# Kernel tuning notes

Measured on AMD Instinct MI355X. Metric: run time of the kernel, lower is better.

The kernel has to match this reference:

```python
import jax, jax.numpy as jnp
import numpy as np

POOL_H, POOL_W = 7, 7


def _crop_and_resize_one(feat, boxes, pool_h, pool_w):
    """TF crop_and_resize-style bilinear sampling.
    feat: [H, W, C]; boxes: [N, 4] normalized (y1, x1, y2, x2).
    Returns [N, pool_h, pool_w, C].
    """
    H, W, C = feat.shape
    y1, x1, y2, x2 = boxes[:, 0], boxes[:, 1], boxes[:, 2], boxes[:, 3]
    fy = jnp.arange(pool_h, dtype=feat.dtype) / (pool_h - 1)  # [ph] in [0,1]
    fx = jnp.arange(pool_w, dtype=feat.dtype) / (pool_w - 1)  # [pw]
    ys = (y1[:, None] + fy[None, :] * (y2 - y1)[:, None]) * (H - 1)  # [N, ph]
    xs = (x1[:, None] + fx[None, :] * (x2 - x1)[:, None]) * (W - 1)  # [N, pw]
    y0f = jnp.clip(jnp.floor(ys), 0, H - 1)
    x0f = jnp.clip(jnp.floor(xs), 0, W - 1)
    y0 = y0f.astype(jnp.int32)
    x0 = x0f.astype(jnp.int32)
    y1i = jnp.clip(y0 + 1, 0, H - 1)
    x1i = jnp.clip(x0 + 1, 0, W - 1)
    wy = (ys - y0f)[:, :, None, None]  # [N, ph, 1, 1]
    wx = (xs - x0f)[:, None, :, None]  # [N, 1, pw, 1]
    # four corner gathers -> [N, ph, pw, C]
    f00 = feat[y0[:, :, None], x0[:, None, :]]
    f01 = feat[y0[:, :, None], x1i[:, None, :]]
    f10 = feat[y1i[:, :, None], x0[:, None, :]]
    f11 = feat[y1i[:, :, None], x1i[:, None, :]]
    top = f00 + (f01 - f00) * wx
    bot = f10 + (f11 - f10) * wx
    return top + (bot - top) * wy


def setup_inputs() -> dict:
    key = jax.random.key(0)
    kf, kb = jax.random.split(key)
    B, H, W, C, N = 2, 64, 64, 256, 2000
    features = jax.random.normal(kf, (B, H, W, C), dtype=jnp.float32)
    p = jax.random.uniform(kb, (B, N, 4), dtype=jnp.float32)
    # ensure valid normalized boxes (y1<=y2, x1<=x2)
    rois = jnp.stack([
        jnp.minimum(p[..., 0], p[..., 2]),
        jnp.minimum(p[..., 1], p[..., 3]),
        jnp.maximum(p[..., 0], p[..., 2]),
        jnp.maximum(p[..., 1], p[..., 3]),
    ], axis=-1)
    return {"features": features, "rois": rois}


def reference(features, rois):
    # [B, N, 7, 7, C]
    return jax.vmap(lambda f, b: _crop_and_resize_one(f, b, POOL_H, POOL_W))(features, rois)
```

## Files before the change

### kernel.cpp

```cpp
#include <hip/hip_runtime.h>


#define POOL  7
#define NBINS 128
#define CAP   14000
#define BPB   8

typedef float vfloat4 __attribute__((ext_vector_type(4)));

__global__ void zero_counts(int* __restrict__ counts) {
    if ((int)threadIdx.x < NBINS) counts[threadIdx.x] = 0;
}

__global__ __launch_bounds__(256) void bin_rows(
    const float* __restrict__ rois,
    int* __restrict__ counts,
    int* __restrict__ slots,
    int H, int N)
{
    const int rows_per_batch = N * POOL;
    const int total = 2 * rows_per_batch;
    const int gid = blockIdx.x * 256 + threadIdx.x;
    if (gid >= total) return;

    const int b   = gid / rows_per_batch;
    const int rem = gid - b * rows_per_batch;
    const int n   = rem / POOL;
    const int py  = rem - n * POOL;

    const float* r = rois + ((long long)b * N + n) * 4;
    const float ry1 = r[0], ry2 = r[2];

    const float fy  = (float)py * (1.0f / (POOL - 1));
    const float ys  = (ry1 + fy * (ry2 - ry1)) * (float)(H - 1);
    const float y0f = fminf(fmaxf(floorf(ys), 0.0f), (float)(H - 1));
    const int   y0  = (int)y0f;

    const int bin = b * 64 + y0;
    const int idx = atomicAdd(&counts[bin], 1);
    slots[bin * CAP + idx] = rem;
}

__global__ __launch_bounds__(1024) void roialign_binned(
    const float* __restrict__ feat,
    const float* __restrict__ rois,
    float* __restrict__ out,
    const int* __restrict__ counts,
    const int* __restrict__ slots,
    int H, int W, int C4, int N)
{
    __shared__ vfloat4 lds[2][64 * 64];

    const int bin = blockIdx.x >> 3;
    const int j   = blockIdx.x & (BPB - 1);
    const int count = counts[bin];
    const int s0 = (j * count) / BPB;
    const int s1 = ((j + 1) * count) / BPB;
    if (s0 >= s1) return;

    const int b   = bin >> 6;
    const int y0  = bin & 63;
    const int y1i = min(y0 + 1, H - 1);

    const vfloat4* fb = (const vfloat4*)feat + (long long)b * H * W * C4;
    const vfloat4* g0 = fb + (long long)y0  * W * C4;
    const vfloat4* g1 = fb + (long long)y1i * W * C4;
    for (int t = threadIdx.x; t < W * C4; t += 1024) {
        lds[0][t] = g0[t];
        lds[1][t] = g1[t];
    }
    __syncthreads();

    const int lane = threadIdx.x & 63;
    const int wid  = threadIdx.x >> 6;

    for (int i = s0 + wid; i < s1; i += 16) {
        const int rem = slots[bin * CAP + i];
        const int n   = rem / POOL;
        const int py  = rem - n * POOL;

        const float* r = rois + ((long long)b * N + n) * 4;
        const float ry1 = r[0], rx1 = r[1], ry2 = r[2], rx2 = r[3];

        const float fy  = (float)py * (1.0f / (POOL - 1));
        const float ys  = (ry1 + fy * (ry2 - ry1)) * (float)(H - 1);
        const float y0f = fminf(fmaxf(floorf(ys), 0.0f), (float)(H - 1));
        const float wy  = ys - y0f;
        const float dx  = rx2 - rx1;

        vfloat4* ob = (vfloat4*)out +
            (((long long)b * N + n) * (POOL * POOL) + (long long)py * POOL) * C4 + lane;

#pragma unroll
        for (int px = 0; px < POOL; ++px) {
            const float fx  = (float)px * (1.0f / (POOL - 1));
            const float xs  = (rx1 + fx * dx) * (float)(W - 1);
            const float x0f = fminf(fmaxf(floorf(xs), 0.0f), (float)(W - 1));
            const int   x0  = (int)x0f;
            const int   x1i = min(x0 + 1, W - 1);
            const float wx  = xs - x0f;

            const vfloat4 f00 = lds[0][x0  * C4 + lane];
            const vfloat4 f01 = lds[0][x1i * C4 + lane];
            const vfloat4 f10 = lds[1][x0  * C4 + lane];
            const vfloat4 f11 = lds[1][x1i * C4 + lane];

            const vfloat4 top = f00 + (f01 - f00) * wx;
            const vfloat4 bot = f10 + (f11 - f10) * wx;
            const vfloat4 o   = top + (bot - top) * wy;

            __builtin_nontemporal_store(o, ob + px * C4);
        }
    }
}

__global__ __launch_bounds__(256) void roialign_direct(
    const float* __restrict__ feat, const float* __restrict__ rois,
    float* __restrict__ out, int H, int W, int C4, int N, int blocks_per_batch)
{
    const int lane = threadIdx.x & 63;
    const int wid  = threadIdx.x >> 6;
    const int xcd  = blockIdx.x & 7;
    const int slot = blockIdx.x >> 3;
    const int b    = xcd >> 2;
    const int lblock = slot * 4 + (xcd & 3);
    if (lblock >= blocks_per_batch) return;
    const int row = lblock * 4 + wid;
    if (row >= N * POOL) return;
    const int n  = row / POOL;
    const int py = row - n * POOL;

    const float* r = rois + ((long long)b * N + n) * 4;
    const float ry1 = r[0], rx1 = r[1], ry2 = r[2], rx2 = r[3];
    const float fy  = (float)py * (1.0f / (POOL - 1));
    const float ys  = (ry1 + fy * (ry2 - ry1)) * (float)(H - 1);
    const float y0f = fminf(fmaxf(floorf(ys), 0.0f), (float)(H - 1));
    const int   y0  = (int)y0f;
    const int   y1i = min(y0 + 1, H - 1);
    const float wy  = ys - y0f;

    const vfloat4* fb = (const vfloat4*)feat + (long long)b * H * W * C4;
    const vfloat4* r0 = fb + (long long)y0  * W * C4 + lane;
    const vfloat4* r1 = fb + (long long)y1i * W * C4 + lane;
    vfloat4* ob = (vfloat4*)out +
        (((long long)b * N + n) * (POOL * POOL) + (long long)py * POOL) * C4 + lane;
    const float dx = rx2 - rx1;
#pragma unroll
    for (int px = 0; px < POOL; ++px) {
        const float fx  = (float)px * (1.0f / (POOL - 1));
        const float xs  = (rx1 + fx * dx) * (float)(W - 1);
        const float x0f = fminf(fmaxf(floorf(xs), 0.0f), (float)(W - 1));
        const int   x0  = (int)x0f;
        const int   x1i = min(x0 + 1, W - 1);
        const float wx  = xs - x0f;
        const vfloat4 f00 = r0[x0  * C4];
        const vfloat4 f01 = r0[x1i * C4];
        const vfloat4 f10 = r1[x0  * C4];
        const vfloat4 f11 = r1[x1i * C4];
        const vfloat4 top = f00 + (f01 - f00) * wx;
        const vfloat4 bot = f10 + (f11 - f10) * wx;
        const vfloat4 o   = top + (bot - top) * wy;
        __builtin_nontemporal_store(o, ob + px * C4);
    }
}

extern "C" void kernel_launch(void* const* d_in, const int* in_sizes, int n_in,
                              void* d_out, int out_size, void* d_ws, size_t ws_size,
                              hipStream_t stream) {
    const int B = 2, H = 64, W = 64, C = 256;
    const int N = in_sizes[1] / (B * 4);

    const float* feat = (const float*)d_in[0];
    const float* rois = (const float*)d_in[1];
    float* out = (float*)d_out;

    const size_t ws_needed = (size_t)NBINS * 4
                           + (size_t)NBINS * CAP * 4;

    if (ws_size >= ws_needed && d_ws != nullptr) {
        int* counts = (int*)d_ws;
        int* slots  = counts + NBINS;

        const int total_rows = B * N * POOL;
        const int bin_blocks = (total_rows + 255) / 256;

        zero_counts<<<1, NBINS, 0, stream>>>(counts);
        bin_rows<<<bin_blocks, 256, 0, stream>>>(rois, counts, slots, H, N);
        roialign_binned<<<NBINS * BPB, 1024, 0, stream>>>(
            feat, rois, out, counts, slots, H, W, C / 4, N);
    } else {
        const int rows_per_batch   = N * POOL;
        const int blocks_per_batch = (rows_per_batch + 3) / 4;
        const int slots_g  = (blocks_per_batch + 3) / 4;
        roialign_direct<<<slots_g * 8, 256, 0, stream>>>(
            feat, rois, out, H, W, C / 4, N, blocks_per_batch);
    }
}
```

Baseline: 245.3 us.

## Replace LDS-staged binned kernel with sorted-row global-gather kernel via prefix scan

Drops the per-bin LDS staging of two feature rows. Each wavefront now handles one output row, found through a prefix-scanned offset table and a binary search over bins, so rows that share a y0 run next to each other and hit the same feature rows in L2. A 40 KB dummy shared array caps occupancy, presumably to keep concurrent wavefronts on nearby bins. The cost is an extra scan kernel plus a binary search per wave, in exchange for removing the LDS load phase and the load imbalance across bins.

```diff
diff --git a/kernel.cpp b/kernel.cpp
--- a/kernel.cpp
+++ b/kernel.cpp
@@ -3,8 +3,6 @@
 
 #define POOL  7
 #define NBINS 128
-#define CAP   14000
-#define BPB   8
 
 typedef float vfloat4 __attribute__((ext_vector_type(4)));
 
@@ -16,7 +14,7 @@
     const float* __restrict__ rois,
     int* __restrict__ counts,
     int* __restrict__ slots,
-    int H, int N)
+    int H, int N, int CAP)
 {
     const int rows_per_batch = N * POOL;
     const int total = 2 * rows_per_batch;
@@ -41,76 +39,88 @@
     slots[bin * CAP + idx] = rem;
 }
 
-__global__ __launch_bounds__(1024) void roialign_binned(
+__global__ void prefix_scan(const int* __restrict__ counts,
+                            int* __restrict__ offsets) {
+    __shared__ int tmp[NBINS];
+    const int t = threadIdx.x;
+    tmp[t] = counts[t];
+    __syncthreads();
+    for (int d = 1; d < NBINS; d <<= 1) {
+        const int v = (t >= d) ? tmp[t - d] : 0;
+        __syncthreads();
+        tmp[t] += v;
+        __syncthreads();
+    }
+    offsets[t + 1] = tmp[t];
+    if (t == 0) offsets[0] = 0;
+}
+
+__global__ __launch_bounds__(256) void roialign_sorted(
     const float* __restrict__ feat,
     const float* __restrict__ rois,
     float* __restrict__ out,
-    const int* __restrict__ counts,
+    const int* __restrict__ offsets,
     const int* __restrict__ slots,
-    int H, int W, int C4, int N)
+    int H, int W, int C4, int N, int CAP, int total)
 {
-    __shared__ vfloat4 lds[2][64 * 64];
-
-    const int bin = blockIdx.x >> 3;
-    const int j   = blockIdx.x & (BPB - 1);
-    const int count = counts[bin];
-    const int s0 = (j * count) / BPB;
-    const int s1 = ((j + 1) * count) / BPB;
-    if (s0 >= s1) return;
-
-    const int b   = bin >> 6;
-    const int y0  = bin & 63;
-    const int y1i = min(y0 + 1, H - 1);
-
-    const vfloat4* fb = (const vfloat4*)feat + (long long)b * H * W * C4;
-    const vfloat4* g0 = fb + (long long)y0  * W * C4;
-    const vfloat4* g1 = fb + (long long)y1i * W * C4;
-    for (int t = threadIdx.x; t < W * C4; t += 1024) {
-        lds[0][t] = g0[t];
-        lds[1][t] = g1[t];
-    }
-    __syncthreads();
+    __shared__ int occ_pad[10240];
+    if (H == 0) ((volatile int*)occ_pad)[threadIdx.x] = 1;
 
     const int lane = threadIdx.x & 63;
     const int wid  = threadIdx.x >> 6;
-
-    for (int i = s0 + wid; i < s1; i += 16) {
-        const int rem = slots[bin * CAP + i];
-        const int n   = rem / POOL;
-        const int py  = rem - n * POOL;
-
-        const float* r = rois + ((long long)b * N + n) * 4;
-        const float ry1 = r[0], rx1 = r[1], ry2 = r[2], rx2 = r[3];
-
-        const float fy  = (float)py * (1.0f / (POOL - 1));
-        const float ys  = (ry1 + fy * (ry2 - ry1)) * (float)(H - 1);
-        const float y0f = fminf(fmaxf(floorf(ys), 0.0f), (float)(H - 1));
-        const float wy  = ys - y0f;
-        const float dx  = rx2 - rx1;
-
-        vfloat4* ob = (vfloat4*)out +
-            (((long long)b * N + n) * (POOL * POOL) + (long long)py * POOL) * C4 + lane;
+    const int gid  = blockIdx.x * 4 + wid;
+    if (gid >= total) return;
+
+    int lo = 0, hi = NBINS;
+    while (hi - lo > 1) {
+        const int mid = (lo + hi) >> 1;
+        if (offsets[mid] <= gid) lo = mid; else hi = mid;
+    }
+    const int bin = lo;
+    const int rem = slots[bin * CAP + (gid - offsets[lo])];
+    const int b   = bin >> 6;
+
+    const int n  = rem / POOL;
+    const int py = rem - n * POOL;
+
+    const float* r = rois + ((long long)b * N + n) * 4;
+    const float ry1 = r[0], rx1 = r[1], ry2 = r[2], rx2 = r[3];
+
+    const float fy  = (float)py * (1.0f / (POOL - 1));
+    const float ys  = (ry1 + fy * (ry2 - ry1)) * (float)(H - 1);
+    const float y0f = fminf(fmaxf(floorf(ys), 0.0f), (float)(H - 1));
+    const int   y0  = (int)y0f;
+    const int   y1i = min(y0 + 1, H - 1);
+    const float wy  = ys - y0f;
+
+    const vfloat4* fb = (const vfloat4*)feat + (long long)b * H * W * C4;
+    const vfloat4* r0 = fb + (long long)y0  * W * C4 + lane;
+    const vfloat4* r1 = fb + (long long)y1i * W * C4 + lane;
+
+    vfloat4* ob = (vfloat4*)out +
+        (((long long)b * N + n) * (POOL * POOL) + (long long)py * POOL) * C4 + lane;
+
+    const float dx = rx2 - rx1;
 
 #pragma unroll
-        for (int px = 0; px < POOL; ++px) {
-            const float fx  = (float)px * (1.0f / (POOL - 1));
-            const float xs  = (rx1 + fx * dx) * (float)(W - 1);
-            const float x0f = fminf(fmaxf(floorf(xs), 0.0f), (float)(W - 1));
-            const int   x0  = (int)x0f;
-            const int   x1i = min(x0 + 1, W - 1);
-            const float wx  = xs - x0f;
-
-            const vfloat4 f00 = lds[0][x0  * C4 + lane];
-            const vfloat4 f01 = lds[0][x1i * C4 + lane];
-            const vfloat4 f10 = lds[1][x0  * C4 + lane];
-            const vfloat4 f11 = lds[1][x1i * C4 + lane];
-
-            const vfloat4 top = f00 + (f01 - f00) * wx;
-            const vfloat4 bot = f10 + (f11 - f10) * wx;
-            const vfloat4 o   = top + (bot - top) * wy;
-
-            __builtin_nontemporal_store(o, ob + px * C4);
-        }
+    for (int px = 0; px < POOL; ++px) {
+        const float fx  = (float)px * (1.0f / (POOL - 1));
+        const float xs  = (rx1 + fx * dx) * (float)(W - 1);
+        const float x0f = fminf(fmaxf(floorf(xs), 0.0f), (float)(W - 1));
+        const int   x0  = (int)x0f;
+        const int   x1i = min(x0 + 1, W - 1);
+        const float wx  = xs - x0f;
+
+        const vfloat4 f00 = r0[x0  * C4];
+        const vfloat4 f01 = r0[x1i * C4];
+        const vfloat4 f10 = r1[x0  * C4];
+        const vfloat4 f11 = r1[x1i * C4];
+
+        const vfloat4 top = f00 + (f01 - f00) * wx;
+        const vfloat4 bot = f10 + (f11 - f10) * wx;
+        const vfloat4 o   = top + (bot - top) * wy;
+
+        __builtin_nontemporal_store(o, ob + px * C4);
     }
 }
 
@@ -174,24 +184,29 @@
     const float* rois = (const float*)d_in[1];
     float* out = (float*)d_out;
 
-    const size_t ws_needed = (size_t)NBINS * 4
+    const int rows_per_batch = N * POOL;
+    const int CAP   = rows_per_batch;
+    const int total = B * rows_per_batch;
+
+    const size_t ws_needed = 512 * 4
                            + (size_t)NBINS * CAP * 4;
 
     if (ws_size >= ws_needed && d_ws != nullptr) {
-        int* counts = (int*)d_ws;
-        int* slots  = counts + NBINS;
-
-        const int total_rows = B * N * POOL;
-        const int bin_blocks = (total_rows + 255) / 256;
+        int* counts  = (int*)d_ws;
+        int* offsets = counts + 128;
+        int* slots   = counts + 512;
+
+        const int bin_blocks = (total + 255) / 256;
+        const int con_blocks = (total + 3) / 4;
 
         zero_counts<<<1, NBINS, 0, stream>>>(counts);
-        bin_rows<<<bin_blocks, 256, 0, stream>>>(rois, counts, slots, H, N);
-        roialign_binned<<<NBINS * BPB, 1024, 0, stream>>>(
-            feat, rois, out, counts, slots, H, W, C / 4, N);
+        bin_rows<<<bin_blocks, 256, 0, stream>>>(rois, counts, slots, H, N, CAP);
+        prefix_scan<<<1, NBINS, 0, stream>>>(counts, offsets);
+        roialign_sorted<<<con_blocks, 256, 0, stream>>>(
+            feat, rois, out, offsets, slots, H, W, C / 4, N, CAP, total);
     } else {
-        const int rows_per_batch   = N * POOL;
         const int blocks_per_batch = (rows_per_batch + 3) / 4;
-        const int slots_g  = (blocks_per_batch + 3) / 4;
+        const int slots_g = (blocks_per_batch + 3) / 4;
         roialign_direct<<<slots_g * 8, 256, 0, stream>>>(
             feat, rois, out, H, W, C / 4, N, blocks_per_batch);
     }
```

New measurement: 269.1 us. 9.7% more time.
